# Optimization experiments

Measured on AMD Instinct MI355X. Metric: run time of the kernel, lower is better.

The kernel has to match this reference:

```python
import jax, jax.numpy as jnp
import numpy as np

TOP_K = 8


def setup_inputs() -> dict:
    key = jax.random.key(0)
    k1, k2 = jax.random.split(key)
    hidden_states = jax.random.normal(k1, (16384, 2048), dtype=jnp.float32)
    weight = jax.random.normal(k2, (64, 2048), dtype=jnp.float32) * 0.02
    return {"hidden_states": hidden_states, "weight": weight}


def reference(hidden_states, weight):
    # router_logits = F.linear(hidden_states, weight): [T, E]
    router_logits = jnp.einsum('th,eh->te', hidden_states, weight)
    # softmax in float32 as in the original
    router_probs = jax.nn.softmax(router_logits.astype(jnp.float32), axis=-1)
    router_top_values, router_indices = jax.lax.top_k(router_probs, TOP_K)
    # norm_topk_prob=True: renormalize selected probs to sum to 1
    router_top_values = router_top_values / jnp.sum(router_top_values, axis=-1, keepdims=True)
    return (router_logits,
            router_top_values.astype(hidden_states.dtype),
            router_indices)
```

## Files before the change

### kernel.cpp

```cpp
#include <hip/hip_runtime.h>
#include <math.h>

#define T_TOKENS 16384
#define HID      2048
#define NE       64
#define TOPK     8
#define TM       32
#define BK       128
#define NCH      (HID / BK)
#define RSTR     272
#define A_SPL    (TM * RSTR)
#define ABUF     (3 * A_SPL)
#define LDS_BYTES (2 * ABUF)

#define WS_LG_OFF   786432
#define WS_NEEDED   (WS_LG_OFF + (size_t)T_TOKENS * NE * 8)

typedef float    f32x4  __attribute__((ext_vector_type(4)));
typedef float    f32x16 __attribute__((ext_vector_type(16)));
typedef short    short8 __attribute__((ext_vector_type(8)));
typedef unsigned uint4v __attribute__((ext_vector_type(4)));

#define MFMA32(A, B, C) __builtin_amdgcn_mfma_f32_32x32x16_bf16((A), (B), (C), 0, 0, 0)

static __device__ __forceinline__ unsigned short f2bf(float x) {
    unsigned u = __builtin_bit_cast(unsigned, x);
    return (unsigned short)((u + 0x7FFFu + ((u >> 16) & 1u)) >> 16);
}

static __device__ __forceinline__ void split8(const float4 v0, const float4 v1,
                                              uint4v& p0, uint4v& p1, uint4v& p2)
{
    const float x[8] = {v0.x, v0.y, v0.z, v0.w, v1.x, v1.y, v1.z, v1.w};
    #pragma unroll
    for (int j = 0; j < 4; ++j) {
        const float xe = x[2 * j], xo = x[2 * j + 1];
        const unsigned ue  = __builtin_bit_cast(unsigned, xe);
        const unsigned m0e = (ue + 0x8000u) & 0xFFFF0000u;
        const float    r1e = xe - __builtin_bit_cast(float, m0e);
        const unsigned u1e = __builtin_bit_cast(unsigned, r1e);
        const unsigned m1e = (u1e + 0x8000u) & 0xFFFF0000u;
        const float    r2e = r1e - __builtin_bit_cast(float, m1e);
        const unsigned u2e = __builtin_bit_cast(unsigned, r2e);
        const unsigned uo  = __builtin_bit_cast(unsigned, xo);
        const unsigned m0o = (uo + 0x8000u) & 0xFFFF0000u;
        const float    r1o = xo - __builtin_bit_cast(float, m0o);
        const unsigned u1o = __builtin_bit_cast(unsigned, r1o);
        const unsigned m1o = (u1o + 0x8000u) & 0xFFFF0000u;
        const float    r2o = r1o - __builtin_bit_cast(float, m1o);
        const unsigned u2o = __builtin_bit_cast(unsigned, r2o);
        p0[j] = m0o | (m0e >> 16);
        p1[j] = m1o | (m1e >> 16);
        p2[j] = (u2o & 0xFFFF0000u) | (u2e >> 16);
    }
}

__global__ __launch_bounds__(256) void split_weight_kernel(
    const float* __restrict__ weight, uint4v* __restrict__ ws)
{
    const int n = blockIdx.x;
    const int o = threadIdx.x;
    const float4 w0 = *(const float4*)&weight[(size_t)n * HID + o * 8];
    const float4 w1 = *(const float4*)&weight[(size_t)n * HID + o * 8 + 4];
    uint4v p0, p1, p2;
    split8(w0, w1, p0, p1, p2);
    const int t   = o >> 1;
    const int idx = t * 128 + (n >> 5) * 64 + (o & 1) * 32 + (n & 31);
    ws[idx]         = p0;
    ws[idx + 16384] = p1;
    ws[idx + 32768] = p2;
}

template<bool FUSED>
__global__ __launch_bounds__(256, 2) void router_kernel(
    const float* __restrict__ hidden,
    const short8* __restrict__ bfrag,
    double* __restrict__ lgws,
    float* __restrict__ out_logits,
    float* __restrict__ out_vals,
    float* __restrict__ out_idxf)
{
    __shared__ __align__(16) char smem[LDS_BYTES];

    const int tid  = threadIdx.x;
    const int tok0 = blockIdx.x * TM;
    const int lane = tid & 63;
    const int wave = tid >> 6;
    const int eh   = wave & 1;
    const int kh   = wave >> 1;

    const int ar   = tid >> 3;
    const int ac16 = (tid & 7) * 16;
    const float* aG = hidden + (size_t)(tok0 + ar) * HID + ac16;
    const int aWOff = ar * RSTR + ac16 * 2;

    const int aOff = (lane & 31) * RSTR + (lane >> 5) * 16 + kh * 128;
    const short8* bP = bfrag + eh * 64 + lane;

    f32x16 acch, accl;
    double accd[16];
    #pragma unroll
    for (int i = 0; i < 16; ++i) { acch[i] = 0.f; accl[i] = 0.f; accd[i] = 0.0; }

    float4 pa[4];

#define STAGE_A(dstbase) do {                                                     \
    uint4v p0_, p1_, p2_;                                                         \
    char* aW_ = (dstbase) + aWOff;                                                \
    split8(pa[0], pa[1], p0_, p1_, p2_);                                          \
    *(uint4v*)(aW_            ) = p0_;                                            \
    *(uint4v*)(aW_ +   A_SPL  ) = p1_;                                            \
    *(uint4v*)(aW_ + 2*A_SPL  ) = p2_;                                            \
    split8(pa[2], pa[3], p0_, p1_, p2_);                                          \
    *(uint4v*)(aW_             + 16) = p0_;                                       \
    *(uint4v*)(aW_ +   A_SPL   + 16) = p1_;                                       \
    *(uint4v*)(aW_ + 2*A_SPL   + 16) = p2_;                                       \
} while (0)

    #pragma unroll
    for (int q = 0; q < 4; ++q) pa[q] = *(const float4*)(aG + 4 * q);
    STAGE_A(smem);
    __syncthreads();

    for (int c = 0; c < NCH; ++c) {
        const char* bufc = smem + (c & 1) * ABUF;

        if (c + 1 < NCH) {
            const int off = (c + 1) * BK;
            #pragma unroll
            for (int q = 0; q < 4; ++q) pa[q] = *(const float4*)(aG + off + 4 * q);
        }

        #pragma unroll
        for (int st = 0; st < 4; ++st) {
            const char* ab = bufc + aOff + st * 32;
            const short8 A0 = *(const short8*)(ab);
            const short8 A1 = *(const short8*)(ab + A_SPL);
            const short8 A2 = *(const short8*)(ab + 2 * A_SPL);
            const int T = (c * 8 + kh * 4 + st) * 128;
            const short8 B0 = bP[T];
            const short8 B1 = bP[T + 16384];
            const short8 B2 = bP[T + 32768];
            acch = MFMA32(A0, B0, acch);
            accl = MFMA32(A0, B1, accl);
            accl = MFMA32(A1, B0, accl);
            accl = MFMA32(A1, B1, accl);
            accl = MFMA32(A0, B2, accl);
            accl = MFMA32(A2, B0, accl);
        }

        #pragma unroll
        for (int i = 0; i < 16; ++i) accd[i] += (double)acch[i];
        #pragma unroll
        for (int i = 0; i < 16; ++i) acch[i] = 0.f;

        if (c + 1 < NCH) {
            STAGE_A(smem + ((c & 1) ^ 1) * ABUF);
        }
        __syncthreads();
    }

    int rowmap[16], colmap[16];
    {
        const unsigned short mb = f2bf((float)(lane & 31));
        const unsigned short ob = f2bf(0.0625f);
        short8 vm, vo;
        #pragma unroll
        for (int j = 0; j < 8; ++j) { vm[j] = (short)mb; vo[j] = (short)ob; }
        f32x16 z;
        #pragma unroll
        for (int i = 0; i < 16; ++i) z[i] = 0.f;
        const f32x16 pr = MFMA32(vm, vo, z);
        const f32x16 pc = MFMA32(vo, vm, z);
        #pragma unroll
        for (int i = 0; i < 16; ++i) {
            rowmap[i] = (int)(pr[i] + 0.5f);
            colmap[i] = (int)(pc[i] + 0.5f);
        }
    }

    double lfin[16];
    #pragma unroll
    for (int i = 0; i < 16; ++i) lfin[i] = accd[i] + (double)accl[i];

    double* red = (double*)smem;
    if (kh == 1) {
        #pragma unroll
        for (int i = 0; i < 16; ++i) red[(eh * 64 + lane) * 17 + i] = lfin[i];
    }
    __syncthreads();

    double (*lg)[NE + 1] = reinterpret_cast<double(*)[NE + 1]>(smem + 17408);

    if (kh == 0) {
        #pragma unroll
        for (int i = 0; i < 16; ++i) {
            lfin[i] += red[(eh * 64 + lane) * 17 + i];
            const int trow = rowmap[i];
            const int tok  = tok0 + trow;
            const int col  = eh * 32 + colmap[i];
            out_logits[(size_t)tok * NE + col] = (float)lfin[i];
            if constexpr (!FUSED) lgws[(size_t)tok * NE + col] = lfin[i];
            else                  lg[trow][col] = lfin[i];
        }
    }

    if constexpr (FUSED) {
        __syncthreads();
        for (int tt = wave; tt < TM; tt += 4) {
            double cur = lg[tt][lane];
            double first = 0.0;
            float  s = 0.f, myv = 0.f;
            int myi = 0;
            #pragma unroll
            for (int i = 0; i < TOPK; ++i) {
                double mv = cur;
                #pragma unroll
                for (int off = 32; off; off >>= 1) {
                    const double ov = __shfl_xor(mv, off);
                    mv = ov > mv ? ov : mv;
                }
                const unsigned long long m = __ballot(cur == mv);
                const int mi = __ffsll(m) - 1;
                if (i == 0) first = mv;
                const float e = expf((float)(mv - first));
                s += e;
                if (lane == i)  { myv = e; myi = mi; }
                if (lane == mi) cur = -INFINITY;
            }
            if (lane < TOPK) {
                const int tok = tok0 + tt;
                out_vals[(size_t)tok * TOPK + lane] = myv / s;
                out_idxf[(size_t)tok * TOPK + lane] = (float)myi;
            }
        }
    }
}

__global__ __launch_bounds__(256) void topk_kernel(
    const double* __restrict__ lgws,
    float* __restrict__ out_vals,
    float* __restrict__ out_idxf)
{
    const int lane = threadIdx.x & 63;
    const int gw   = (blockIdx.x * 256 + threadIdx.x) >> 6;
    for (int tok = gw; tok < T_TOKENS; tok += 4096) {
        double cur = lgws[(size_t)tok * NE + lane];
        double first = 0.0;
        float  s = 0.f, myv = 0.f;
        int myi = 0;
        #pragma unroll
        for (int i = 0; i < TOPK; ++i) {
            double mv = cur;
            #pragma unroll
            for (int off = 32; off; off >>= 1) {
                const double ov = __shfl_xor(mv, off);
                mv = ov > mv ? ov : mv;
            }
            const unsigned long long m = __ballot(cur == mv);
            const int mi = __ffsll(m) - 1;
            if (i == 0) first = mv;
            const float e = expf((float)(mv - first));
            s += e;
            if (lane == i)  { myv = e; myi = mi; }
            if (lane == mi) cur = -INFINITY;
        }
        if (lane < TOPK) {
            out_vals[(size_t)tok * TOPK + lane] = myv / s;
            out_idxf[(size_t)tok * TOPK + lane] = (float)myi;
        }
    }
}

extern "C" void kernel_launch(void* const* d_in, const int* in_sizes, int n_in,
                              void* d_out, int out_size, void* d_ws, size_t ws_size,
                              hipStream_t stream) {
    const float* hidden = (const float*)d_in[0];
    const float* weight = (const float*)d_in[1];

    float* out        = (float*)d_out;
    float* out_logits = out;
    float* out_vals   = out + (size_t)T_TOKENS * NE;
    float* out_idxf   = out + (size_t)T_TOKENS * NE + (size_t)T_TOKENS * TOPK;

    uint4v* ws   = (uint4v*)d_ws;
    double* lgws = (double*)((char*)d_ws + WS_LG_OFF);

    hipLaunchKernelGGL(split_weight_kernel, dim3(NE), dim3(256), 0, stream,
                       weight, ws);

    if (ws_size >= WS_NEEDED) {
        hipLaunchKernelGGL((router_kernel<false>), dim3(T_TOKENS / TM), dim3(256),
                           0, stream, hidden, (const short8*)ws, lgws,
                           out_logits, out_vals, out_idxf);
        hipLaunchKernelGGL(topk_kernel, dim3(1024), dim3(256), 0, stream,
                           lgws, out_vals, out_idxf);
    } else {
        hipLaunchKernelGGL((router_kernel<true>), dim3(T_TOKENS / TM), dim3(256),
                           0, stream, hidden, (const short8*)ws, (double*)nullptr,
                           out_logits, out_vals, out_idxf);
    }
}
```

Before: 233.1 us.

## Drop LDS staging of A and split K across four waves with direct loads

Each wave now loads its own hidden-state fragments straight from global memory, splits them into bf16 parts in registers and feeds the MFMAs directly, so the LDS double buffer and per-chunk barriers are gone. Work is partitioned with each wave covering all 64 experts over a quarter of K, and the partials of three waves are reduced through LDS in double precision. The per-chunk double accumulation of the high product is replaced by one fp32 accumulation over the whole K range. This removes LDS traffic and sync overhead, but loads to registers are less coalesced, each wave reads twice the B fragments, and more accumulator registers are needed.

```diff
diff --git a/kernel.cpp b/kernel.cpp
--- a/kernel.cpp
+++ b/kernel.cpp
@@ -6,17 +6,13 @@
 #define NE       64
 #define TOPK     8
 #define TM       32
-#define BK       128
-#define NCH      (HID / BK)
-#define RSTR     272
-#define A_SPL    (TM * RSTR)
-#define ABUF     (3 * A_SPL)
-#define LDS_BYTES (2 * ABUF)
+#define NSTEP    32
 
 #define WS_LG_OFF   786432
 #define WS_NEEDED   (WS_LG_OFF + (size_t)T_TOKENS * NE * 8)
 
-typedef float    f32x4  __attribute__((ext_vector_type(4)));
+#define LDS_BYTES   50688
+
 typedef float    f32x16 __attribute__((ext_vector_type(16)));
 typedef short    short8 __attribute__((ext_vector_type(8)));
 typedef unsigned uint4v __attribute__((ext_vector_type(4)));
@@ -81,133 +77,119 @@
     float* __restrict__ out_idxf)
 {
     __shared__ __align__(16) char smem[LDS_BYTES];
+    double* red = (double*)smem;
 
     const int tid  = threadIdx.x;
     const int tok0 = blockIdx.x * TM;
     const int lane = tid & 63;
-    const int wave = tid >> 6;
-    const int eh   = wave & 1;
-    const int kh   = wave >> 1;
-
-    const int ar   = tid >> 3;
-    const int ac16 = (tid & 7) * 16;
-    const float* aG = hidden + (size_t)(tok0 + ar) * HID + ac16;
-    const int aWOff = ar * RSTR + ac16 * 2;
-
-    const int aOff = (lane & 31) * RSTR + (lane >> 5) * 16 + kh * 128;
-    const short8* bP = bfrag + eh * 64 + lane;
-
-    f32x16 acch, accl;
-    double accd[16];
+    const int kh   = tid >> 6;
+
+    const int arow = lane & 31;
+    const float* aRow = hidden + (size_t)(tok0 + arow) * HID + (lane >> 5) * 8;
+
+    const short8* bP0 = bfrag + lane;
+    const short8* bP1 = bfrag + 64 + lane;
+
+    f32x16 acch0, acch1, accl0, accl1;
     #pragma unroll
-    for (int i = 0; i < 16; ++i) { acch[i] = 0.f; accl[i] = 0.f; accd[i] = 0.0; }
-
-    float4 pa[4];
-
-#define STAGE_A(dstbase) do {                                                     \
-    uint4v p0_, p1_, p2_;                                                         \
-    char* aW_ = (dstbase) + aWOff;                                                \
-    split8(pa[0], pa[1], p0_, p1_, p2_);                                          \
-    *(uint4v*)(aW_            ) = p0_;                                            \
-    *(uint4v*)(aW_ +   A_SPL  ) = p1_;                                            \
-    *(uint4v*)(aW_ + 2*A_SPL  ) = p2_;                                            \
-    split8(pa[2], pa[3], p0_, p1_, p2_);                                          \
-    *(uint4v*)(aW_             + 16) = p0_;                                       \
-    *(uint4v*)(aW_ +   A_SPL   + 16) = p1_;                                       \
-    *(uint4v*)(aW_ + 2*A_SPL   + 16) = p2_;                                       \
-} while (0)
-
+    for (int i = 0; i < 16; ++i) {
+        acch0[i] = 0.f; acch1[i] = 0.f; accl0[i] = 0.f; accl1[i] = 0.f;
+    }
+
+    #pragma unroll 4
+    for (int s = 0; s < NSTEP; ++s) {
+        const int k = (s >> 1) * 128 + kh * 32 + (s & 1) * 16;
+        const float4 a0 = *(const float4*)(aRow + k);
+        const float4 a1 = *(const float4*)(aRow + k + 4);
+        uint4v p0, p1, p2;
+        split8(a0, a1, p0, p1, p2);
+        const short8 A0 = __builtin_bit_cast(short8, p0);
+        const short8 A1 = __builtin_bit_cast(short8, p1);
+        const short8 A2 = __builtin_bit_cast(short8, p2);
+        const int T = (k >> 4) * 128;
+        const short8 B00 = bP0[T];
+        const short8 B01 = bP0[T + 16384];
+        const short8 B02 = bP0[T + 32768];
+        const short8 B10 = bP1[T];
+        const short8 B11 = bP1[T + 16384];
+        const short8 B12 = bP1[T + 32768];
+        acch0 = MFMA32(A0, B00, acch0);
+        acch1 = MFMA32(A0, B10, acch1);
+        accl0 = MFMA32(A1, B00, accl0);
+        accl1 = MFMA32(A1, B10, accl1);
+        accl0 = MFMA32(A0, B01, accl0);
+        accl1 = MFMA32(A0, B11, accl1);
+        accl0 = MFMA32(A1, B01, accl0);
+        accl1 = MFMA32(A1, B11, accl1);
+        accl0 = MFMA32(A0, B02, accl0);
+        accl1 = MFMA32(A0, B12, accl1);
+        accl0 = MFMA32(A2, B00, accl0);
+        accl1 = MFMA32(A2, B10, accl1);
+    }
+
+    double lf0[16], lf1[16];
     #pragma unroll
-    for (int q = 0; q < 4; ++q) pa[q] = *(const float4*)(aG + 4 * q);
-    STAGE_A(smem);
+    for (int i = 0; i < 16; ++i) {
+        lf0[i] = (double)acch0[i] + (double)accl0[i];
+        lf1[i] = (double)acch1[i] + (double)accl1[i];
+    }
+
+    if (kh != 0) {
+        double* r = red + ((kh - 1) * 64 + lane) * 33;
+        #pragma unroll
+        for (int i = 0; i < 16; ++i) { r[i] = lf0[i]; r[16 + i] = lf1[i]; }
+    }
     __syncthreads();
 
-    for (int c = 0; c < NCH; ++c) {
-        const char* bufc = smem + (c & 1) * ABUF;
-
-        if (c + 1 < NCH) {
-            const int off = (c + 1) * BK;
-            #pragma unroll
-            for (int q = 0; q < 4; ++q) pa[q] = *(const float4*)(aG + off + 4 * q);
-        }
-
-        #pragma unroll
-        for (int st = 0; st < 4; ++st) {
-            const char* ab = bufc + aOff + st * 32;
-            const short8 A0 = *(const short8*)(ab);
-            const short8 A1 = *(const short8*)(ab + A_SPL);
-            const short8 A2 = *(const short8*)(ab + 2 * A_SPL);
-            const int T = (c * 8 + kh * 4 + st) * 128;
-            const short8 B0 = bP[T];
-            const short8 B1 = bP[T + 16384];
-            const short8 B2 = bP[T + 32768];
-            acch = MFMA32(A0, B0, acch);
-            accl = MFMA32(A0, B1, accl);
-            accl = MFMA32(A1, B0, accl);
-            accl = MFMA32(A1, B1, accl);
-            accl = MFMA32(A0, B2, accl);
-            accl = MFMA32(A2, B0, accl);
-        }
-
-        #pragma unroll
-        for (int i = 0; i < 16; ++i) accd[i] += (double)acch[i];
-        #pragma unroll
-        for (int i = 0; i < 16; ++i) acch[i] = 0.f;
-
-        if (c + 1 < NCH) {
-            STAGE_A(smem + ((c & 1) ^ 1) * ABUF);
-        }
-        __syncthreads();
-    }
-
-    int rowmap[16], colmap[16];
-    {
-        const unsigned short mb = f2bf((float)(lane & 31));
-        const unsigned short ob = f2bf(0.0625f);
-        short8 vm, vo;
-        #pragma unroll
-        for (int j = 0; j < 8; ++j) { vm[j] = (short)mb; vo[j] = (short)ob; }
-        f32x16 z;
-        #pragma unroll
-        for (int i = 0; i < 16; ++i) z[i] = 0.f;
-        const f32x16 pr = MFMA32(vm, vo, z);
-        const f32x16 pc = MFMA32(vo, vm, z);
+    if (kh == 0) {
+        #pragma unroll
+        for (int q = 0; q < 3; ++q) {
+            const double* r = red + (q * 64 + lane) * 33;
+            #pragma unroll
+            for (int i = 0; i < 16; ++i) { lf0[i] += r[i]; lf1[i] += r[16 + i]; }
+        }
+
+        int rowmap[16], colmap[16];
+        {
+            const unsigned short mb = f2bf((float)(lane & 31));
+            const unsigned short ob = f2bf(0.0625f);
+            short8 vm, vo;
+            #pragma unroll
+            for (int j = 0; j < 8; ++j) { vm[j] = (short)mb; vo[j] = (short)ob; }
+            f32x16 z;
+            #pragma unroll
+            for (int i = 0; i < 16; ++i) z[i] = 0.f;
+            const f32x16 pr = MFMA32(vm, vo, z);
+            const f32x16 pc = MFMA32(vo, vm, z);
+            #pragma unroll
+            for (int i = 0; i < 16; ++i) {
+                rowmap[i] = (int)(pr[i] + 0.5f);
+                colmap[i] = (int)(pc[i] + 0.5f);
+            }
+        }
+
+        double (*lg)[65] = reinterpret_cast<double(*)[65]>(smem);
         #pragma unroll
         for (int i = 0; i < 16; ++i) {
-            rowmap[i] = (int)(pr[i] + 0.5f);
-            colmap[i] = (int)(pc[i] + 0.5f);
-        }
-    }
-
-    double lfin[16];
-    #pragma unroll
-    for (int i = 0; i < 16; ++i) lfin[i] = accd[i] + (double)accl[i];
-
-    double* red = (double*)smem;
-    if (kh == 1) {
-        #pragma unroll
-        for (int i = 0; i < 16; ++i) red[(eh * 64 + lane) * 17 + i] = lfin[i];
-    }
-    __syncthreads();
-
-    double (*lg)[NE + 1] = reinterpret_cast<double(*)[NE + 1]>(smem + 17408);
-
-    if (kh == 0) {
-        #pragma unroll
-        for (int i = 0; i < 16; ++i) {
-            lfin[i] += red[(eh * 64 + lane) * 17 + i];
             const int trow = rowmap[i];
             const int tok  = tok0 + trow;
-            const int col  = eh * 32 + colmap[i];
-            out_logits[(size_t)tok * NE + col] = (float)lfin[i];
-            if constexpr (!FUSED) lgws[(size_t)tok * NE + col] = lfin[i];
-            else                  lg[trow][col] = lfin[i];
+            const int c0   = colmap[i];
+            out_logits[(size_t)tok * NE + c0]      = (float)lf0[i];
+            out_logits[(size_t)tok * NE + c0 + 32] = (float)lf1[i];
+            if constexpr (!FUSED) {
+                lgws[(size_t)tok * NE + c0]      = lf0[i];
+                lgws[(size_t)tok * NE + c0 + 32] = lf1[i];
+            } else {
+                lg[trow][c0]      = lf0[i];
+                lg[trow][c0 + 32] = lf1[i];
+            }
         }
     }
 
     if constexpr (FUSED) {
         __syncthreads();
-        for (int tt = wave; tt < TM; tt += 4) {
+        double (*lg)[65] = reinterpret_cast<double(*)[65]>(smem);
+        for (int tt = kh; tt < TM; tt += 4) {
             double cur = lg[tt][lane];
             double first = 0.0;
             float  s = 0.f, myv = 0.f;
```

Result: no change. 231.8 us (-0.5%).
